# Kernel optimization log

Hardware: AMD Instinct MI355X
Metric: run time of the kernel (lower is better)

Reference implementation:

```python
import jax, jax.numpy as jnp
import numpy as np

B, T, N, D = 8, 128, 256, 64  # batch, timesteps, nodes, d_model
LN_EPS = 1e-5


def _ln(x, g, b):
    m = x.mean(-1, keepdims=True)
    v = ((x - m) ** 2).mean(-1, keepdims=True)
    return (x - m) / jnp.sqrt(v + LN_EPS) * g + b


def setup_inputs() -> dict:
    key = jax.random.key(0)
    ks = jax.random.split(key, 12)
    s = 0.05
    f32 = jnp.float32
    return {
        "H_i": jax.random.normal(ks[0], (B, T, N, D), dtype=f32),
        "H_j": jax.random.normal(ks[1], (B, T, N, D), dtype=f32),
        # CrossModalTemporalAligner params (torch Linear: y = x @ W.T + b, W is [out,in])
        "Wq": jax.random.normal(ks[2], (D, D), dtype=f32) * s, "bq": jnp.zeros((D,), f32),
        "Wk": jax.random.normal(ks[3], (D, D), dtype=f32) * s, "bk": jnp.zeros((D,), f32),
        "Wv": jax.random.normal(ks[4], (D, D), dtype=f32) * s, "bv": jnp.zeros((D,), f32),
        "log_gamma": jnp.zeros((), f32),
        "log_tau": jnp.zeros((), f32),
        # GCNMambaLayer params
        "e1": jax.random.normal(ks[5], (N, 32), dtype=f32),
        "e2": jax.random.normal(ks[6], (32, N), dtype=f32),
        "Wg": jax.random.normal(ks[7], (D, D), dtype=f32) * s, "bg": jnp.zeros((D,), f32),
        "ln1_g": jnp.ones((D,), f32), "ln1_b": jnp.zeros((D,), f32),
        # GRU fallback for Mamba block (torch nn.GRU: gates order r,z,n)
        "Wih": jax.random.normal(ks[8], (3 * D, D), dtype=f32) * s,
        "Whh": jax.random.normal(ks[9], (3 * D, D), dtype=f32) * s,
        "bih": jnp.zeros((3 * D,), f32), "bhh": jnp.zeros((3 * D,), f32),
        "ln2_g": jnp.ones((D,), f32), "ln2_b": jnp.zeros((D,), f32),
    }


def _aligner(H_i, H_j, Wq, bq, Wk, bk, Wv, bv, log_gamma, log_tau):
    b, Ti, n, d = H_i.shape
    Tj = H_j.shape[1]
    Q = jnp.einsum("btnd,ed->btne", H_i, Wq) + bq
    K = jnp.einsum("btnd,ed->btne", H_j, Wk) + bk
    V = jnp.einsum("btnd,ed->btne", H_j, Wv) + bv
    # per-node temporal attention: [B, N, Ti, Tj]
    tau = jnp.clip(jnp.exp(log_tau), 0.01)
    sim = jnp.einsum("bind,bjnd->bnij", Q, K) / (d ** 0.5 * tau)
    t_i = jnp.arange(Ti, dtype=jnp.float32) / max(Ti - 1, 1)
    t_j = jnp.arange(Tj, dtype=jnp.float32) / max(Tj - 1, 1)
    gamma = jnp.clip(jnp.exp(log_gamma), 0.01)
    decay = jnp.exp(-gamma * jnp.abs(t_i[:, None] - t_j[None, :]))  # [Ti, Tj]
    sim = sim + jnp.log(decay + 1e-8)[None, None]
    attn = jax.nn.softmax(sim, axis=-1)
    out = jnp.einsum("bnij,bjnd->bind", attn, V)  # back to [B, Ti, N, d]
    return out


def _gru(x_tn, Wih, Whh, bih, bhh):
    # x_tn: [B, N, T, d]; scan over T, carry h: [B, N, d]
    d = x_tn.shape[-1]
    xs = jnp.moveaxis(x_tn, 2, 0)  # [T, B, N, d]
    h0 = jnp.zeros(x_tn.shape[:2] + (d,), x_tn.dtype)

    def step(h, x_t):
        gi = x_t @ Wih.T + bih
        gh = h @ Whh.T + bhh
        i_r, i_z, i_n = jnp.split(gi, 3, axis=-1)
        h_r, h_z, h_n = jnp.split(gh, 3, axis=-1)
        r = jax.nn.sigmoid(i_r + h_r)
        z = jax.nn.sigmoid(i_z + h_z)
        n = jnp.tanh(i_n + r * h_n)
        h_new = (1.0 - z) * n + z * h
        return h_new, h_new

    _, outs = jax.lax.scan(step, h0, xs)
    return jnp.moveaxis(outs, 0, 2)  # [B, N, T, d]


def _gcn_mamba(x, e1, e2, Wg, bg, ln1_g, ln1_b, Wih, Whh, bih, bhh, ln2_g, ln2_b):
    # adaptive adjacency: softmax over dim=1 (columns) of relu(e1@e2)
    adp = jax.nn.softmax(jax.nn.relu(e1 @ e2), axis=1)  # [N, N]
    h_gcn = jax.nn.relu(jnp.einsum("mn,btnd->btmd", adp, x) @ Wg.T + bg)
    x = _ln(x + h_gcn, ln1_g, ln1_b)  # dropout is identity in eval
    x_tn = jnp.transpose(x, (0, 2, 1, 3))  # [B, N, T, d]
    ssm_out = _gru(x_tn, Wih, Whh, bih, bhh)
    h_mb = _ln(x_tn + ssm_out, ln2_g, ln2_b)  # MambaTemporalBlock: norm(x + ssm(x))
    x = x + jnp.transpose(h_mb, (0, 2, 1, 3))
    return x


def reference(H_i, H_j, Wq, bq, Wk, bk, Wv, bv, log_gamma, log_tau,
              e1, e2, Wg, bg, ln1_g, ln1_b, Wih, Whh, bih, bhh, ln2_g, ln2_b):
    aligned = _aligner(H_i, H_j, Wq, bq, Wk, bk, Wv, bv, log_gamma, log_tau)
    return _gcn_mamba(aligned, e1, e2, Wg, bg, ln1_g, ln1_b,
                      Wih, Whh, bih, bhh, ln2_g, ln2_b)
```

## Files before the change

### kernel.cpp

```cpp
#include <hip/hip_runtime.h>
#include <cstddef>

#define BB 8
#define TT 128
#define NN 256
#define DD 64

typedef _Float16 half2_t __attribute__((ext_vector_type(2)));
typedef _Float16 half4_t __attribute__((ext_vector_type(4)));
typedef _Float16 half8_t __attribute__((ext_vector_type(8)));
typedef float f32x4 __attribute__((ext_vector_type(4)));

#if defined(__has_builtin)
#  if __has_builtin(__builtin_amdgcn_fdot2)
#    define FDOT2(a,b,c) __builtin_amdgcn_fdot2((a),(b),(c),false)
#  endif
#endif
#ifndef FDOT2
#  define FDOT2(a,b,c) ((c) + (float)(a).x*(float)(b).x + (float)(a).y*(float)(b).y)
#endif

union h8u { half8_t v; half2_t h[4]; };

__device__ __forceinline__ float wave64_sum(float x) {
#if defined(__has_builtin) && __has_builtin(__builtin_amdgcn_update_dpp)
  int t;
  t = __builtin_amdgcn_update_dpp(0, __builtin_bit_cast(int, x), 0x111, 0xF, 0xF, true);
  x += __builtin_bit_cast(float, t);
  t = __builtin_amdgcn_update_dpp(0, __builtin_bit_cast(int, x), 0x112, 0xF, 0xF, true);
  x += __builtin_bit_cast(float, t);
  t = __builtin_amdgcn_update_dpp(0, __builtin_bit_cast(int, x), 0x114, 0xF, 0xF, true);
  x += __builtin_bit_cast(float, t);
  t = __builtin_amdgcn_update_dpp(0, __builtin_bit_cast(int, x), 0x118, 0xF, 0xF, true);
  x += __builtin_bit_cast(float, t);
  float g0 = __builtin_bit_cast(float, __builtin_amdgcn_readlane(__builtin_bit_cast(int, x), 15));
  float g1 = __builtin_bit_cast(float, __builtin_amdgcn_readlane(__builtin_bit_cast(int, x), 31));
  float g2 = __builtin_bit_cast(float, __builtin_amdgcn_readlane(__builtin_bit_cast(int, x), 47));
  float g3 = __builtin_bit_cast(float, __builtin_amdgcn_readlane(__builtin_bit_cast(int, x), 63));
  return (g0 + g1) + (g2 + g3);
#else
  #pragma unroll
  for (int off = 32; off > 0; off >>= 1) x += __shfl_xor(x, off, 64);
  return x;
#endif
}

__global__ __launch_bounds__(256) void k_prep(
    const float* __restrict__ Wq, const float* __restrict__ Wk, const float* __restrict__ Wv,
    const float* __restrict__ Wg,
    unsigned int* __restrict__ wq2, unsigned int* __restrict__ wk2,
    unsigned int* __restrict__ wv2, unsigned int* __restrict__ wg2)
{
  int t = blockIdx.x * 256 + threadIdx.x;
  if (t < 2048) {
    half2_t a; a.x = (_Float16)Wq[2*t]; a.y = (_Float16)Wq[2*t+1];
    wq2[t] = __builtin_bit_cast(unsigned int, a);
    half2_t b; b.x = (_Float16)Wk[2*t]; b.y = (_Float16)Wk[2*t+1];
    wk2[t] = __builtin_bit_cast(unsigned int, b);
    half2_t c; c.x = (_Float16)Wv[2*t]; c.y = (_Float16)Wv[2*t+1];
    wv2[t] = __builtin_bit_cast(unsigned int, c);
    half2_t d; d.x = (_Float16)Wg[2*t]; d.y = (_Float16)Wg[2*t+1];
    wg2[t] = __builtin_bit_cast(unsigned int, d);
  }
}

#define KSTR 72
#define PSTR 136

__device__ __forceinline__ half8_t wfrag(const unsigned int* __restrict__ W2, int e, int k0) {
  return *(const half8_t*)(W2 + e * 32 + (k0 >> 1));
}

__global__ __launch_bounds__(256, 2) void k_attn(
    const float* __restrict__ Hi, const float* __restrict__ Hj,
    const unsigned int* __restrict__ wq2, const unsigned int* __restrict__ wk2,
    const unsigned int* __restrict__ wv2,
    const float* __restrict__ bq, const float* __restrict__ bk, const float* __restrict__ bv,
    const float* __restrict__ lgp, const float* __restrict__ ltp,
    float* __restrict__ out)
{
  __shared__ __align__(16) _Float16 sK[TT][KSTR];
  __shared__ __align__(16) _Float16 sVt[DD][PSTR];
  __shared__ __align__(16) _Float16 sP[4][32][PSTR];
  __shared__ float sDecay[TT];

  const int b   = blockIdx.x >> 8;
  const int n   = blockIdx.x & 255;
  const int tid = threadIdx.x;
  const int w   = tid >> 6;
  const int l   = tid & 63;
  const int l16 = l & 15;
  const int lg4 = l >> 4;

  const float gamma = fmaxf(__expf(lgp[0]), 0.01f);
  const float tau   = fmaxf(__expf(ltp[0]), 0.01f);
  const float scale = 1.0f / (8.0f * tau);
  if (tid < TT) {
    float dt = gamma * (float)tid * (1.0f / 127.0f);
    sDecay[tid] = __logf(__expf(-dt) + 1e-8f);
  }

  const int row0 = 32 * w;
  half8_t hai[2][2], haj[2][2];
  #pragma unroll
  for (int mt = 0; mt < 2; mt++) {
    const int i = row0 + 16 * mt + l16;
    const float* ri = Hi + (((size_t)b * TT + i) * NN + n) * DD;
    const float* rj = Hj + (((size_t)b * TT + i) * NN + n) * DD;
    #pragma unroll
    for (int ks = 0; ks < 2; ks++) {
      const int k0 = 32 * ks + 8 * lg4;
      float4 a = *(const float4*)(ri + k0);
      float4 c = *(const float4*)(ri + k0 + 4);
      half8_t h;
      h[0]=(_Float16)a.x; h[1]=(_Float16)a.y; h[2]=(_Float16)a.z; h[3]=(_Float16)a.w;
      h[4]=(_Float16)c.x; h[5]=(_Float16)c.y; h[6]=(_Float16)c.z; h[7]=(_Float16)c.w;
      hai[mt][ks] = h;
      a = *(const float4*)(rj + k0);
      c = *(const float4*)(rj + k0 + 4);
      h[0]=(_Float16)a.x; h[1]=(_Float16)a.y; h[2]=(_Float16)a.z; h[3]=(_Float16)a.w;
      h[4]=(_Float16)c.x; h[5]=(_Float16)c.y; h[6]=(_Float16)c.z; h[7]=(_Float16)c.w;
      haj[mt][ks] = h;
    }
  }

  #pragma unroll
  for (int nt = 0; nt < 4; nt++) {
    const int e = 16 * nt + l16;
    half8_t wb0 = wfrag(wq2, e, 8 * lg4);
    half8_t wb1 = wfrag(wq2, e, 32 + 8 * lg4);
    const float be = bq[e];
    #pragma unroll
    for (int mt = 0; mt < 2; mt++) {
      f32x4 acc = {be, be, be, be};
      acc = __builtin_amdgcn_mfma_f32_16x16x32_f16(hai[mt][0], wb0, acc, 0, 0, 0);
      acc = __builtin_amdgcn_mfma_f32_16x16x32_f16(hai[mt][1], wb1, acc, 0, 0, 0);
      #pragma unroll
      for (int r = 0; r < 4; r++)
        sP[w][16 * mt + 4 * lg4 + r][e] = (_Float16)(acc[r] * scale);
    }
  }

  #pragma unroll
  for (int nt = 0; nt < 4; nt++) {
    const int e = 16 * nt + l16;
    half8_t wb0 = wfrag(wk2, e, 8 * lg4);
    half8_t wb1 = wfrag(wk2, e, 32 + 8 * lg4);
    const float be = bk[e];
    #pragma unroll
    for (int mt = 0; mt < 2; mt++) {
      f32x4 acc = {be, be, be, be};
      acc = __builtin_amdgcn_mfma_f32_16x16x32_f16(haj[mt][0], wb0, acc, 0, 0, 0);
      acc = __builtin_amdgcn_mfma_f32_16x16x32_f16(haj[mt][1], wb1, acc, 0, 0, 0);
      #pragma unroll
      for (int r = 0; r < 4; r++)
        sK[row0 + 16 * mt + 4 * lg4 + r][e] = (_Float16)acc[r];
    }
  }

  #pragma unroll
  for (int nt = 0; nt < 4; nt++) {
    const int e = 16 * nt + l16;
    half8_t wb0 = wfrag(wv2, e, 8 * lg4);
    half8_t wb1 = wfrag(wv2, e, 32 + 8 * lg4);
    const float be = bv[e];
    #pragma unroll
    for (int mt = 0; mt < 2; mt++) {
      f32x4 acc = {be, be, be, be};
      acc = __builtin_amdgcn_mfma_f32_16x16x32_f16(haj[mt][0], wb0, acc, 0, 0, 0);
      acc = __builtin_amdgcn_mfma_f32_16x16x32_f16(haj[mt][1], wb1, acc, 0, 0, 0);
      const int jb = row0 + 16 * mt + 4 * lg4;
      half4_t v4;
      v4[0] = (_Float16)acc[0]; v4[1] = (_Float16)acc[1];
      v4[2] = (_Float16)acc[2]; v4[3] = (_Float16)acc[3];
      *(half4_t*)(&sVt[e][jb]) = v4;
    }
  }
  __syncthreads();

  half8_t qa[2][2];
  #pragma unroll
  for (int mt = 0; mt < 2; mt++)
    #pragma unroll
    for (int ks = 0; ks < 2; ks++)
      qa[mt][ks] = *(const half8_t*)(&sP[w][16 * mt + l16][32 * ks + 8 * lg4]);

  float rs[2][4] = {{0.f,0.f,0.f,0.f},{0.f,0.f,0.f,0.f}};
  for (int jt = 0; jt < 8; jt++) {
    const int j = 16 * jt + l16;
    half8_t kb0 = *(const half8_t*)(&sK[j][8 * lg4]);
    half8_t kb1 = *(const half8_t*)(&sK[j][32 + 8 * lg4]);
    #pragma unroll
    for (int mt = 0; mt < 2; mt++) {
      f32x4 acc = {0.f, 0.f, 0.f, 0.f};
      acc = __builtin_amdgcn_mfma_f32_16x16x32_f16(qa[mt][0], kb0, acc, 0, 0, 0);
      acc = __builtin_amdgcn_mfma_f32_16x16x32_f16(qa[mt][1], kb1, acc, 0, 0, 0);
      #pragma unroll
      for (int r = 0; r < 4; r++) {
        const int il = 16 * mt + 4 * lg4 + r;
        int di = (row0 + il) - j; di = di < 0 ? -di : di;
        float p = __expf(acc[r] + sDecay[di]);
        rs[mt][r] += p;
        sP[w][il][j] = (_Float16)p;
      }
    }
  }

  f32x4 oacc[2][4] = {};
  #pragma unroll
  for (int ks = 0; ks < 4; ks++) {
    const int j0 = 32 * ks + 8 * lg4;
    half8_t pa0 = *(const half8_t*)(&sP[w][l16][j0]);
    half8_t pa1 = *(const half8_t*)(&sP[w][16 + l16][j0]);
    #pragma unroll
    for (int nt = 0; nt < 4; nt++) {
      half8_t vb = *(const half8_t*)(&sVt[16 * nt + l16][j0]);
      oacc[0][nt] = __builtin_amdgcn_mfma_f32_16x16x32_f16(pa0, vb, oacc[0][nt], 0, 0, 0);
      oacc[1][nt] = __builtin_amdgcn_mfma_f32_16x16x32_f16(pa1, vb, oacc[1][nt], 0, 0, 0);
    }
  }

  #pragma unroll
  for (int mt = 0; mt < 2; mt++)
    #pragma unroll
    for (int r = 0; r < 4; r++) {
      float v = rs[mt][r];
      v += __shfl_xor(v, 1, 64);
      v += __shfl_xor(v, 2, 64);
      v += __shfl_xor(v, 4, 64);
      v += __shfl_xor(v, 8, 64);
      rs[mt][r] = 1.0f / v;
    }
  #pragma unroll
  for (int mt = 0; mt < 2; mt++) {
    #pragma unroll
    for (int r = 0; r < 4; r++) {
      const int i = row0 + 16 * mt + 4 * lg4 + r;
      float* orow = out + (((size_t)b * TT + i) * NN + n) * DD;
      const float rl = rs[mt][r];
      #pragma unroll
      for (int nt = 0; nt < 4; nt++)
        orow[16 * nt + l16] = oacc[mt][nt][r] * rl;
    }
  }
}

__global__ __launch_bounds__(256) void k_adp(
    const float* __restrict__ e1, const float* __restrict__ e2,
    unsigned short* __restrict__ adph)
{
  const int m = blockIdx.x, n = threadIdx.x;
  float s = 0.f;
  #pragma unroll
  for (int k = 0; k < 32; k++) s += e1[m*32+k] * e2[k*256+n];
  s = fmaxf(s, 0.f);
  __shared__ float red[256];
  red[n] = s; __syncthreads();
  for (int off = 128; off > 0; off >>= 1) {
    if (n < off) red[n] = fmaxf(red[n], red[n+off]);
    __syncthreads();
  }
  float mx = red[0];
  __syncthreads();
  float p = __expf(s - mx);
  red[n] = p; __syncthreads();
  for (int off = 128; off > 0; off >>= 1) {
    if (n < off) red[n] += red[n+off];
    __syncthreads();
  }
  _Float16 h = (_Float16)(p / red[0]);
  adph[m*256 + n] = __builtin_bit_cast(unsigned short, h);
}

#define GSTR 280

__global__ __launch_bounds__(256, 2) void k_gcn(
    float* __restrict__ x, const unsigned short* __restrict__ adph,
    const unsigned int* __restrict__ wg2, const float* __restrict__ bg,
    const float* __restrict__ g1, const float* __restrict__ b1)
{
  __shared__ __align__(16) _Float16 sxhT[DD][GSTR];
  __shared__ __align__(16) _Float16 sgT[DD][GSTR];

  const int tid = threadIdx.x;
  const int w   = tid >> 6;
  const int l   = tid & 63;
  const int l16 = l & 15;
  const int lg4 = l >> 4;
  float* tile = x + (size_t)blockIdx.x * NN * DD;

  {
    const int d2 = tid & 31;
    const int mg = tid >> 5;
    #pragma unroll
    for (int it = 0; it < 16; it++) {
      const int m0 = mg * 2 + it * 16;
      float2 va = *(const float2*)(tile + (size_t)m0 * DD + 2 * d2);
      float2 vb = *(const float2*)(tile + (size_t)(m0 + 1) * DD + 2 * d2);
      half2_t h0; h0.x = (_Float16)va.x; h0.y = (_Float16)vb.x;
      half2_t h1; h1.x = (_Float16)va.y; h1.y = (_Float16)vb.y;
      *(half2_t*)(&sxhT[2 * d2][m0])     = h0;
      *(half2_t*)(&sxhT[2 * d2 + 1][m0]) = h1;
    }
  }
  __syncthreads();

  f32x4 acc1[4][4] = {};
  for (int ks = 0; ks < 8; ks++) {
    const int k0 = 32 * ks + 8 * lg4;
    half8_t bfr[4], afr[4];
    #pragma unroll
    for (int nt = 0; nt < 4; nt++)
      bfr[nt] = *(const half8_t*)(&sxhT[16 * nt + l16][k0]);
    #pragma unroll
    for (int mt = 0; mt < 4; mt++) {
      const int m = 64 * w + 16 * mt + l16;
      afr[mt] = *(const half8_t*)(adph + m * 256 + k0);
    }
    #pragma unroll
    for (int mt = 0; mt < 4; mt++)
      #pragma unroll
      for (int nt = 0; nt < 4; nt++)
        acc1[mt][nt] = __builtin_amdgcn_mfma_f32_16x16x32_f16(afr[mt], bfr[nt], acc1[mt][nt], 0, 0, 0);
  }

  #pragma unroll
  for (int mt = 0; mt < 4; mt++)
    #pragma unroll
    for (int nt = 0; nt < 4; nt++) {
      half4_t g4;
      g4[0] = (_Float16)acc1[mt][nt][0]; g4[1] = (_Float16)acc1[mt][nt][1];
      g4[2] = (_Float16)acc1[mt][nt][2]; g4[3] = (_Float16)acc1[mt][nt][3];
      *(half4_t*)(&sgT[16 * nt + l16][64 * w + 16 * mt + 4 * lg4]) = g4;
    }
  __syncthreads();

  half8_t wb[4][2];
  float bgv[4], g1v[4], b1v[4];
  #pragma unroll
  for (int et = 0; et < 4; et++) {
    const int e = 16 * et + l16;
    wb[et][0] = wfrag(wg2, e, 8 * lg4);
    wb[et][1] = wfrag(wg2, e, 32 + 8 * lg4);
    bgv[et] = bg[e]; g1v[et] = g1[e]; b1v[et] = b1[e];
  }

  #pragma unroll 1
  for (int mt = 0; mt < 4; mt++) {
    half8_t ga[2];
    #pragma unroll
    for (int ks = 0; ks < 2; ks++) {
      half8_t h;
      #pragma unroll
      for (int j = 0; j < 8; j++)
        h[j] = sgT[32 * ks + 8 * lg4 + j][64 * w + 16 * mt + l16];
      ga[ks] = h;
    }
    f32x4 acc2[4];
    #pragma unroll
    for (int et = 0; et < 4; et++) {
      f32x4 a = {bgv[et], bgv[et], bgv[et], bgv[et]};
      a = __builtin_amdgcn_mfma_f32_16x16x32_f16(ga[0], wb[et][0], a, 0, 0, 0);
      a = __builtin_amdgcn_mfma_f32_16x16x32_f16(ga[1], wb[et][1], a, 0, 0, 0);
      acc2[et] = a;
    }
    #pragma unroll
    for (int r = 0; r < 4; r++) {
      const int mrow = 64 * w + 16 * mt + 4 * lg4 + r;
      float* xr = tile + (size_t)mrow * DD;
      float y[4], s1 = 0.f, s2 = 0.f;
      #pragma unroll
      for (int et = 0; et < 4; et++) {
        float h = fmaxf(acc2[et][r], 0.f);
        float yv = xr[16 * et + l16] + h;
        y[et] = yv; s1 += yv; s2 += yv * yv;
      }
      #pragma unroll
      for (int off = 1; off < 16; off <<= 1) {
        s1 += __shfl_xor(s1, off, 64);
        s2 += __shfl_xor(s2, off, 64);
      }
      const float mean = s1 * (1.f / 64.f);
      const float var  = fmaxf(s2 * (1.f / 64.f) - mean * mean, 0.f);
      const float rstd = rsqrtf(var + 1e-5f);
      #pragma unroll
      for (int et = 0; et < 4; et++)
        xr[16 * et + l16] = (y[et] - mean) * rstd * g1v[et] + b1v[et];
    }
  }
}

__global__ __launch_bounds__(256) void k_gih(
    const float* __restrict__ x, const float* __restrict__ Wih,
    const float* __restrict__ bih, unsigned int* __restrict__ GI2)
{
  __shared__ unsigned int sW[192*32];
  __shared__ unsigned int sbuf[256*33];
  const int tid = threadIdx.x;
  const int b = blockIdx.x >> 7, t = blockIdx.x & 127;
  const float* xt = x + (((size_t)b * TT + t) * NN) * DD;

  for (int idx = tid; idx < 192*32; idx += 256) {
    float2 w = ((const float2*)Wih)[idx];
    half2_t h; h.x = (_Float16)w.x; h.y = (_Float16)w.y;
    sW[idx] = __builtin_bit_cast(unsigned int, h);
  }
  for (int idx = tid; idx < 256*32; idx += 256) {
    int n = idx >> 5, k = idx & 31;
    float2 v = ((const float2*)xt)[idx];
    half2_t h; h.x = (_Float16)v.x; h.y = (_Float16)v.y;
    sbuf[n*33 + k] = __builtin_bit_cast(unsigned int, h);
  }
  __syncthreads();
  half2_t xr[32];
  #pragma unroll
  for (int k = 0; k < 32; k++) xr[k] = __builtin_bit_cast(half2_t, sbuf[tid*33 + k]);
  __syncthreads();

  const size_t blockbase = ((size_t)t * 2048 + b * 256) * 96;
  for (int c = 0; c < 4; c++) {
    #pragma unroll 2
    for (int j2 = 0; j2 < 24; j2++) {
      int e0 = c*48 + 2*j2;
      float a0 = bih[e0], a1 = bih[e0+1];
      const half8_t* w0 = (const half8_t*)(sW + e0*32);
      const half8_t* w1 = (const half8_t*)(sW + (e0+1)*32);
      #pragma unroll
      for (int kq = 0; kq < 8; kq++) {
        h8u ua, ub; ua.v = w0[kq]; ub.v = w1[kq];
        #pragma unroll
        for (int m = 0; m < 4; m++) {
          a0 = FDOT2(ua.h[m], xr[4*kq+m], a0);
          a1 = FDOT2(ub.h[m], xr[4*kq+m], a1);
        }
      }
      half2_t o; o.x = (_Float16)a0; o.y = (_Float16)a1;
      sbuf[tid*25 + j2] = __builtin_bit_cast(unsigned int, o);
    }
    __syncthreads();
    for (int idx = tid; idx < 6144; idx += 256) {
      int n = idx / 24, e2 = idx % 24;
      GI2[blockbase + (size_t)n*96 + c*24 + e2] = sbuf[n*25 + e2];
    }
    __syncthreads();
  }
}

__global__ __launch_bounds__(256, 2) void k_gru_gi(
    float* __restrict__ x, const _Float16* __restrict__ GIh,
    const float* __restrict__ Whh, const float* __restrict__ bhh,
    const float* __restrict__ g2, const float* __restrict__ b2)
{
  const int tid = threadIdx.x;
  const int w = tid >> 6;
  const int l = tid & 63;
  const int b = blockIdx.x >> 6, n4 = blockIdx.x & 63;

  half2_t wr[32], wz[32], wn[32];
  {
    float2 tmp[32];
    const float2* W0 = (const float2*)(Whh + (size_t)l * 64);
    #pragma unroll
    for (int q = 0; q < 32; q++) tmp[q] = W0[q];
    #pragma unroll
    for (int k = 0; k < 32; k++) {
      float lo = (k & 1) ? tmp[k >> 1].y : tmp[k >> 1].x;
      float hi = (k & 1) ? tmp[16 + (k >> 1)].y : tmp[16 + (k >> 1)].x;
      half2_t h; h.x = (_Float16)lo; h.y = (_Float16)hi; wr[k] = h;
    }
    const float2* W1 = (const float2*)(Whh + (size_t)(64 + l) * 64);
    #pragma unroll
    for (int q = 0; q < 32; q++) tmp[q] = W1[q];
    #pragma unroll
    for (int k = 0; k < 32; k++) {
      float lo = (k & 1) ? tmp[k >> 1].y : tmp[k >> 1].x;
      float hi = (k & 1) ? tmp[16 + (k >> 1)].y : tmp[16 + (k >> 1)].x;
      half2_t h; h.x = (_Float16)lo; h.y = (_Float16)hi; wz[k] = h;
    }
    const float2* W2 = (const float2*)(Whh + (size_t)(128 + l) * 64);
    #pragma unroll
    for (int q = 0; q < 32; q++) tmp[q] = W2[q];
    #pragma unroll
    for (int k = 0; k < 32; k++) {
      float lo = (k & 1) ? tmp[k >> 1].y : tmp[k >> 1].x;
      float hi = (k & 1) ? tmp[16 + (k >> 1)].y : tmp[16 + (k >> 1)].x;
      half2_t h; h.x = (_Float16)lo; h.y = (_Float16)hi; wn[k] = h;
    }
  }
  const float bhr = bhh[l], bhz = bhh[64 + l], bhn = bhh[128 + l];
  const float lng = g2[l], lnb = b2[l];

  float hreg = 0.f;
  unsigned int h2pack = 0;

  const size_t gistride = (size_t)2048 * 192;
  const size_t xstride  = (size_t)NN * DD;
  size_t gioff = ((size_t)b * 256 + n4 * 4 + w) * 192 + l;
  size_t xoff  = (((size_t)b * TT) * NN + n4 * 4 + w) * DD + l;

  float gir = (float)GIh[gioff];
  float giz = (float)GIh[gioff + 64];
  float gin = (float)GIh[gioff + 128];
  float xv  = x[xoff];

  for (int t = 0; t < TT; t++) {
    const size_t adv = (t + 1 < TT) ? 1 : 0;
    const size_t gioff_n = gioff + adv * gistride;
    const size_t xoff_n  = xoff  + adv * xstride;
    float gir_n = (float)GIh[gioff_n];
    float giz_n = (float)GIh[gioff_n + 64];
    float gin_n = (float)GIh[gioff_n + 128];
    float xv_n  = x[xoff_n];

    float ar = bhr, az = bhz, an = bhn;
    #pragma unroll
    for (int k = 0; k < 32; k++) {
      half2_t s2 = __builtin_bit_cast(half2_t,
                     __builtin_amdgcn_readlane((int)h2pack, k));
      ar = FDOT2(wr[k], s2, ar);
      az = FDOT2(wz[k], s2, az);
      an = FDOT2(wn[k], s2, an);
    }

    const float r = 1.f / (1.f + __expf(-(gir + ar)));
    const float z = 1.f / (1.f + __expf(-(giz + az)));
    const float e = __expf(2.f * (gin + r * an));
    const float nt = 1.f - 2.f / (e + 1.f);
    const float hn = (1.f - z) * nt + z * hreg;
    hreg = hn;

    const float other = __shfl_xor(hn, 32, 64);
    const float plo = (l < 32) ? hn : other;
    const float phi = (l < 32) ? other : hn;
    half2_t hp; hp.x = (_Float16)plo; hp.y = (_Float16)phi;
    h2pack = __builtin_bit_cast(unsigned int, hp);

    const float yv = xv + hn;
    const float s1  = wave64_sum(yv);
    const float s2v = wave64_sum(yv * yv);
    const float mean = s1 * 0.015625f;
    const float var  = fmaxf(s2v * 0.015625f - mean * mean, 0.f);
    const float hm = (yv - mean) * rsqrtf(var + 1e-5f) * lng + lnb;
    x[xoff] = xv + hm;

    gir = gir_n; giz = giz_n; gin = gin_n; xv = xv_n;
    gioff += gistride; xoff += xstride;
  }
}

__global__ __launch_bounds__(256) void k_gru(
    float* __restrict__ x,
    const float* __restrict__ Wih, const float* __restrict__ Whh,
    const float* __restrict__ bih, const float* __restrict__ bhh,
    const float* __restrict__ g2, const float* __restrict__ b2)
{
  __shared__ half2_t sWi[192][33];
  __shared__ half2_t sWh[192][33];
  __shared__ float   xs[4][64];
  __shared__ half2_t xs_h[4][32];
  __shared__ float   hs_f[4][64];
  __shared__ half2_t hs_h[4][32];
  __shared__ float   gis[4][192];
  __shared__ float   ghs[4][192];

  const int b  = blockIdx.x >> 6;
  const int ng = blockIdx.x & 63;

  for (int idx = threadIdx.x; idx < 192 * 32; idx += 256) {
    int g = idx >> 5, dh = idx & 31;
    half2_t hv; hv.x = (_Float16)Wih[g*64 + 2*dh]; hv.y = (_Float16)Wih[g*64 + 2*dh + 1];
    sWi[g][dh] = hv;
    half2_t hw; hw.x = (_Float16)Whh[g*64 + 2*dh]; hw.y = (_Float16)Whh[g*64 + 2*dh + 1];
    sWh[g][dh] = hw;
  }
  const int s_d = threadIdx.x >> 6;
  const int d_d = threadIdx.x & 63;
  hs_f[s_d][d_d] = 0.f;
  ((_Float16*)hs_h[s_d])[d_d] = (_Float16)0.f;
  const float lng = g2[d_d], lnb = b2[d_d];

  int   tsk_s[3], tsk_g[3];
  float tb_i[3], tb_h[3];
  #pragma unroll
  for (int k = 0; k < 3; k++) {
    int task = threadIdx.x + k * 256;
    tsk_s[k] = task / 192; tsk_g[k] = task % 192;
    tb_i[k] = bih[tsk_g[k]]; tb_h[k] = bhh[tsk_g[k]];
  }
  __syncthreads();

  const size_t base = (((size_t)b * TT) * NN + ng * 4) * DD;
  for (int t = 0; t < TT; t++) {
    const size_t row = base + (size_t)t * NN * DD + s_d * 64 + d_d;
    float xv = x[row];
    xs[s_d][d_d] = xv;
    ((_Float16*)xs_h[s_d])[d_d] = (_Float16)xv;
    __syncthreads();

    #pragma unroll
    for (int k = 0; k < 3; k++) {
      int s = tsk_s[k], g = tsk_g[k];
      float ai = tb_i[k], ah = tb_h[k];
      #pragma unroll
      for (int dh = 0; dh < 32; dh++) {
        ai = FDOT2(sWi[g][dh], xs_h[s][dh], ai);
        ah = FDOT2(sWh[g][dh], hs_h[s][dh], ah);
      }
      gis[s][g] = ai; ghs[s][g] = ah;
    }
    __syncthreads();

    float gr = gis[s_d][d_d]      + ghs[s_d][d_d];
    float gz = gis[s_d][64 + d_d] + ghs[s_d][64 + d_d];
    float r  = 1.f / (1.f + __expf(-gr));
    float z  = 1.f / (1.f + __expf(-gz));
    float nn = tanhf(gis[s_d][128 + d_d] + r * ghs[s_d][128 + d_d]);
    float ho = hs_f[s_d][d_d];
    float hn = (1.f - z) * nn + z * ho;

    float yv = xs[s_d][d_d] + hn;
    float s1 = yv, s2 = yv * yv;
    #pragma unroll
    for (int off = 32; off > 0; off >>= 1) {
      s1 += __shfl_xor(s1, off, 64);
      s2 += __shfl_xor(s2, off, 64);
    }
    float mean = s1 * (1.f / 64.f);
    float var  = fmaxf(s2 * (1.f / 64.f) - mean * mean, 0.f);
    float hm = (yv - mean) * rsqrtf(var + 1e-5f) * lng + lnb;

    x[row] = xs[s_d][d_d] + hm;
    hs_f[s_d][d_d] = hn;
    ((_Float16*)hs_h[s_d])[d_d] = (_Float16)hn;
    __syncthreads();
  }
}

extern "C" void kernel_launch(void* const* d_in, const int* in_sizes, int n_in,
                              void* d_out, int out_size, void* d_ws, size_t ws_size,
                              hipStream_t stream) {
  const float* Hi  = (const float*)d_in[0];
  const float* Hj  = (const float*)d_in[1];
  const float* Wq  = (const float*)d_in[2];  const float* bq = (const float*)d_in[3];
  const float* Wk  = (const float*)d_in[4];  const float* bk = (const float*)d_in[5];
  const float* Wv  = (const float*)d_in[6];  const float* bv = (const float*)d_in[7];
  const float* lg  = (const float*)d_in[8];  const float* lt = (const float*)d_in[9];
  const float* e1  = (const float*)d_in[10]; const float* e2 = (const float*)d_in[11];
  const float* Wg  = (const float*)d_in[12]; const float* bg = (const float*)d_in[13];
  const float* g1  = (const float*)d_in[14]; const float* b1 = (const float*)d_in[15];
  const float* Wih = (const float*)d_in[16]; const float* Whh = (const float*)d_in[17];
  const float* bih = (const float*)d_in[18]; const float* bhh = (const float*)d_in[19];
  const float* g2  = (const float*)d_in[20]; const float* b2  = (const float*)d_in[21];
  float* out  = (float*)d_out;

  unsigned short* adph = (unsigned short*)d_ws;
  unsigned int* wg2 = (unsigned int*)d_ws + 32768;
  unsigned int* wq2 = (unsigned int*)d_ws + 65536;
  unsigned int* wk2 = wq2 + 2048;
  unsigned int* wv2 = wk2 + 2048;
  const size_t gi_off = 286720;
  const size_t gi_bytes = (size_t)2048 * TT * 192 * 2;
  const bool use_gi = ws_size >= gi_off + gi_bytes;
  unsigned int* GI2 = (unsigned int*)((char*)d_ws + gi_off);
  _Float16*     GIh = (_Float16*)((char*)d_ws + gi_off);

  k_prep<<<dim3(8),     dim3(256), 0, stream>>>(Wq, Wk, Wv, Wg, wq2, wk2, wv2, wg2);
  k_attn<<<dim3(BB*NN), dim3(256), 0, stream>>>(Hi, Hj, wq2, wk2, wv2, bq, bk, bv, lg, lt, out);
  k_adp <<<dim3(NN),    dim3(256), 0, stream>>>(e1, e2, adph);
  k_gcn <<<dim3(BB*TT), dim3(256), 0, stream>>>(out, adph, wg2, bg, g1, b1);
  if (use_gi) {
    k_gih   <<<dim3(BB*TT), dim3(256), 0, stream>>>(out, Wih, bih, GI2);
    k_gru_gi<<<dim3(512),   dim3(256), 0, stream>>>(out, GIh, Whh, bhh, g2, b2);
  } else {
    k_gru   <<<dim3(512),   dim3(256), 0, stream>>>(out, Wih, Whh, bih, bhh, g2, b2);
  }
}
```

Measured before the change: 521.6 us.

## Rewrite input-gate projection kernel with MFMA and pre-converted fp16 weights

```diff
diff --git a/kernel.cpp b/kernel.cpp
--- a/kernel.cpp
+++ b/kernel.cpp
@@ -47,9 +47,10 @@
 
 __global__ __launch_bounds__(256) void k_prep(
     const float* __restrict__ Wq, const float* __restrict__ Wk, const float* __restrict__ Wv,
-    const float* __restrict__ Wg,
+    const float* __restrict__ Wg, const float* __restrict__ Wih,
     unsigned int* __restrict__ wq2, unsigned int* __restrict__ wk2,
-    unsigned int* __restrict__ wv2, unsigned int* __restrict__ wg2)
+    unsigned int* __restrict__ wv2, unsigned int* __restrict__ wg2,
+    unsigned int* __restrict__ wih2)
 {
   int t = blockIdx.x * 256 + threadIdx.x;
   if (t < 2048) {
@@ -61,6 +62,10 @@
     wv2[t] = __builtin_bit_cast(unsigned int, c);
     half2_t d; d.x = (_Float16)Wg[2*t]; d.y = (_Float16)Wg[2*t+1];
     wg2[t] = __builtin_bit_cast(unsigned int, d);
+  }
+  if (t < 6144) {
+    half2_t h; h.x = (_Float16)Wih[2*t]; h.y = (_Float16)Wih[2*t+1];
+    wih2[t] = __builtin_bit_cast(unsigned int, h);
   }
 }
 
@@ -390,59 +395,51 @@
   }
 }
 
-__global__ __launch_bounds__(256) void k_gih(
-    const float* __restrict__ x, const float* __restrict__ Wih,
-    const float* __restrict__ bih, unsigned int* __restrict__ GI2)
+__global__ __launch_bounds__(256, 4) void k_gih(
+    const float* __restrict__ x, const unsigned int* __restrict__ wih2,
+    const float* __restrict__ bih, _Float16* __restrict__ GIh)
 {
-  __shared__ unsigned int sW[192*32];
-  __shared__ unsigned int sbuf[256*33];
   const int tid = threadIdx.x;
+  const int w   = tid >> 6;
+  const int l   = tid & 63;
+  const int l16 = l & 15;
+  const int lg4 = l >> 4;
   const int b = blockIdx.x >> 7, t = blockIdx.x & 127;
-  const float* xt = x + (((size_t)b * TT + t) * NN) * DD;
-
-  for (int idx = tid; idx < 192*32; idx += 256) {
-    float2 w = ((const float2*)Wih)[idx];
-    half2_t h; h.x = (_Float16)w.x; h.y = (_Float16)w.y;
-    sW[idx] = __builtin_bit_cast(unsigned int, h);
-  }
-  for (int idx = tid; idx < 256*32; idx += 256) {
-    int n = idx >> 5, k = idx & 31;
-    float2 v = ((const float2*)xt)[idx];
-    half2_t h; h.x = (_Float16)v.x; h.y = (_Float16)v.y;
-    sbuf[n*33 + k] = __builtin_bit_cast(unsigned int, h);
-  }
-  __syncthreads();
-  half2_t xr[32];
-  #pragma unroll
-  for (int k = 0; k < 32; k++) xr[k] = __builtin_bit_cast(half2_t, sbuf[tid*33 + k]);
-  __syncthreads();
-
-  const size_t blockbase = ((size_t)t * 2048 + b * 256) * 96;
-  for (int c = 0; c < 4; c++) {
-    #pragma unroll 2
-    for (int j2 = 0; j2 < 24; j2++) {
-      int e0 = c*48 + 2*j2;
-      float a0 = bih[e0], a1 = bih[e0+1];
-      const half8_t* w0 = (const half8_t*)(sW + e0*32);
-      const half8_t* w1 = (const half8_t*)(sW + (e0+1)*32);
-      #pragma unroll
-      for (int kq = 0; kq < 8; kq++) {
-        h8u ua, ub; ua.v = w0[kq]; ub.v = w1[kq];
-        #pragma unroll
-        for (int m = 0; m < 4; m++) {
-          a0 = FDOT2(ua.h[m], xr[4*kq+m], a0);
-          a1 = FDOT2(ub.h[m], xr[4*kq+m], a1);
-        }
-      }
-      half2_t o; o.x = (_Float16)a0; o.y = (_Float16)a1;
-      sbuf[tid*25 + j2] = __builtin_bit_cast(unsigned int, o);
-    }
-    __syncthreads();
-    for (int idx = tid; idx < 6144; idx += 256) {
-      int n = idx / 24, e2 = idx % 24;
-      GI2[blockbase + (size_t)n*96 + c*24 + e2] = sbuf[n*25 + e2];
-    }
-    __syncthreads();
+
+  half8_t xb[4][2];
+  #pragma unroll
+  for (int nt = 0; nt < 4; nt++) {
+    const int n = 64 * w + 16 * nt + l16;
+    const float* xr = x + (((size_t)b * TT + t) * NN + n) * DD;
+    #pragma unroll
+    for (int ks = 0; ks < 2; ks++) {
+      const int k0 = 32 * ks + 8 * lg4;
+      float4 a = *(const float4*)(xr + k0);
+      float4 c = *(const float4*)(xr + k0 + 4);
+      half8_t h;
+      h[0]=(_Float16)a.x; h[1]=(_Float16)a.y; h[2]=(_Float16)a.z; h[3]=(_Float16)a.w;
+      h[4]=(_Float16)c.x; h[5]=(_Float16)c.y; h[6]=(_Float16)c.z; h[7]=(_Float16)c.w;
+      xb[nt][ks] = h;
+    }
+  }
+
+  _Float16* gout = GIh + ((size_t)t * 2048 + b * 256 + 64 * w) * 192;
+
+  #pragma unroll 4
+  for (int et = 0; et < 12; et++) {
+    half8_t wa0 = wfrag(wih2, 16 * et + l16, 8 * lg4);
+    half8_t wa1 = wfrag(wih2, 16 * et + l16, 32 + 8 * lg4);
+    float4 bb = *(const float4*)(bih + 16 * et + 4 * lg4);
+    #pragma unroll
+    for (int nt = 0; nt < 4; nt++) {
+      f32x4 acc = {bb.x, bb.y, bb.z, bb.w};
+      acc = __builtin_amdgcn_mfma_f32_16x16x32_f16(wa0, xb[nt][0], acc, 0, 0, 0);
+      acc = __builtin_amdgcn_mfma_f32_16x16x32_f16(wa1, xb[nt][1], acc, 0, 0, 0);
+      half4_t o;
+      o[0] = (_Float16)acc[0]; o[1] = (_Float16)acc[1];
+      o[2] = (_Float16)acc[2]; o[3] = (_Float16)acc[3];
+      *(half4_t*)(gout + (size_t)(16 * nt + l16) * 192 + 16 * et + 4 * lg4) = o;
+    }
   }
 }
 
@@ -654,22 +651,22 @@
   float* out  = (float*)d_out;
 
   unsigned short* adph = (unsigned short*)d_ws;
-  unsigned int* wg2 = (unsigned int*)d_ws + 32768;
-  unsigned int* wq2 = (unsigned int*)d_ws + 65536;
-  unsigned int* wk2 = wq2 + 2048;
-  unsigned int* wv2 = wk2 + 2048;
-  const size_t gi_off = 286720;
+  unsigned int* wg2  = (unsigned int*)d_ws + 32768;
+  unsigned int* wq2  = (unsigned int*)d_ws + 65536;
+  unsigned int* wk2  = wq2 + 2048;
+  unsigned int* wv2  = wk2 + 2048;
+  unsigned int* wih2 = (unsigned int*)d_ws + 71680;
+  const size_t gi_off = 311296;
   const size_t gi_bytes = (size_t)2048 * TT * 192 * 2;
   const bool use_gi = ws_size >= gi_off + gi_bytes;
-  unsigned int* GI2 = (unsigned int*)((char*)d_ws + gi_off);
-  _Float16*     GIh = (_Float16*)((char*)d_ws + gi_off);
-
-  k_prep<<<dim3(8),     dim3(256), 0, stream>>>(Wq, Wk, Wv, Wg, wq2, wk2, wv2, wg2);
+  _Float16* GIh = (_Float16*)((char*)d_ws + gi_off);
+
+  k_prep<<<dim3(24),    dim3(256), 0, stream>>>(Wq, Wk, Wv, Wg, Wih, wq2, wk2, wv2, wg2, wih2);
   k_attn<<<dim3(BB*NN), dim3(256), 0, stream>>>(Hi, Hj, wq2, wk2, wv2, bq, bk, bv, lg, lt, out);
   k_adp <<<dim3(NN),    dim3(256), 0, stream>>>(e1, e2, adph);
   k_gcn <<<dim3(BB*TT), dim3(256), 0, stream>>>(out, adph, wg2, bg, g1, b1);
   if (use_gi) {
-    k_gih   <<<dim3(BB*TT), dim3(256), 0, stream>>>(out, Wih, bih, GI2);
+    k_gih   <<<dim3(BB*TT), dim3(256), 0, stream>>>(out, wih2, bih, GIh);
     k_gru_gi<<<dim3(512),   dim3(256), 0, stream>>>(out, GIh, Whh, bhh, g2, b2);
   } else {
     k_gru   <<<dim3(512),   dim3(256), 0, stream>>>(out, Wih, Whh, bih, bhh, g2, b2);
```

New measurement: 447.3 us. -14.2%, faster.
